# Optimization experiments

Hardware: AMD Instinct MI355X
Metric: run time of the kernel (lower is better)

Reference implementation:

```python
import jax, jax.numpy as jnp
import numpy as np

BLK = 128            # weight_block_size for w8a16 blockwise dequant
H = 1024             # hidden_size
I = 512              # moe_intermediate_size
E = 64               # n_routed_experts
T = 512              # tokens (seq_len)
K = 6                # num_experts_per_tok
G = 8                # n_group
TG = 3               # topk_group
NSH = 2              # n_shared_experts
I2 = I * NSH         # shared expert intermediate size
ROUTED_SCALE = 2.5
NORM_TOPK = True


def dq(w_int8, scale, blk=BLK):
    """Blockwise w8a16 dequant: w [..., M, N] int8, scale [..., M/blk, N/blk] f32."""
    *lead, M, N = w_int8.shape
    w = w_int8.astype(scale.dtype).reshape(*lead, M // blk, blk, N // blk, blk)
    return (w * scale[..., :, None, :, None]).reshape(*lead, M, N)


def setup_inputs() -> dict:
    key = jax.random.key(0)
    ks = jax.random.split(key, 16)
    ri = lambda k, shp: jax.random.randint(k, shp, -8, 8, dtype=jnp.int8)
    rs = lambda k, shp: jax.random.uniform(k, shp, minval=0.01, maxval=0.03, dtype=jnp.float32)
    return {
        "x": jax.random.normal(ks[0], (T, H), jnp.float32),
        "gate_w": jax.random.normal(ks[1], (E, H), jnp.float32) * 0.02,  # router gate [E,H]
        "wg": ri(ks[2], (E, I, H)),  "sg": rs(ks[3], (E, I // BLK, H // BLK)),
        "wu": ri(ks[4], (E, I, H)),  "su": rs(ks[5], (E, I // BLK, H // BLK)),
        "wd": ri(ks[6], (E, I, H)),  "sd": rs(ks[7], (E, I // BLK, H // BLK)),  # down, transposed layout [I,H]
        "sh_wg": ri(ks[8], (I2, H)),  "sh_sg": rs(ks[9], (I2 // BLK, H // BLK)),
        "sh_wu": ri(ks[10], (I2, H)), "sh_su": rs(ks[11], (I2 // BLK, H // BLK)),
        "sh_wd": ri(ks[12], (I2, H)), "sh_sd": rs(ks[13], (I2 // BLK, H // BLK)),
    }


def _moe(x, gate_w, wg, sg, wu, su, wd, sd, sh_wg, sh_sg, sh_wu, sh_su, sh_wd, sh_sd):
    Tn = x.shape[0]
    # --- router: sigmoid scoring + group-limited top-k ---
    scores = jax.nn.sigmoid(x @ gate_w.T)                       # [T, E]
    gsz = E // G
    group_scores = scores.reshape(Tn, G, gsz).max(axis=-1)      # [T, G]
    _, gidx = jax.lax.top_k(group_scores, TG)                   # [T, TG]
    gmask = jax.nn.one_hot(gidx, G, dtype=scores.dtype).sum(1)  # [T, G]
    emask = jnp.repeat(gmask, gsz, axis=-1)                     # [T, E]
    masked = jnp.where(emask > 0, scores, -jnp.inf)
    w, idx = jax.lax.top_k(masked, K)                           # [T, K]
    if NORM_TOPK:
        w = w / (w.sum(-1, keepdims=True) + 1e-20)
    w = w * ROUTED_SCALE
    # per-token combine weights over experts
    comb = (jax.nn.one_hot(idx, E, dtype=x.dtype) * w[:, :, None]).sum(1)  # [T, E]

    # --- routed experts: dequantized silu-gated MLPs, masked dense combine ---
    Wg, Wu, Wd = dq(wg, sg), dq(wu, su), dq(wd, sd)             # [E, I, H]
    g = jnp.einsum('th,eih->eti', x, Wg)                        # [E, T, I]
    u = jnp.einsum('th,eih->eti', x, Wu)
    hmid = jax.nn.silu(g) * u
    y = jnp.einsum('eti,eih->eth', hmid, Wd)                    # [E, T, H]
    routed = jnp.einsum('eth,te->th', y, comb)                  # [T, H]

    # --- shared experts MLP ---
    Sg, Su, Sd = dq(sh_wg, sh_sg), dq(sh_wu, sh_su), dq(sh_wd, sh_sd)
    shared = (jax.nn.silu(x @ Sg.T) * (x @ Su.T)) @ Sd          # [T, H]
    return routed + shared


def reference(x, gate_w, wg, sg, wu, su, wd, sd, sh_wg, sh_sg, sh_wu, sh_su, sh_wd, sh_sd):
    return _moe(x, gate_w, wg, sg, wu, su, wd, sd,
                sh_wg, sh_sg, sh_wu, sh_su, sh_wd, sh_sd)
```

## Files before the change

kernel.cpp:

```cpp
#include <hip/hip_runtime.h>
#include <math.h>
#include <stdint.h>

#define T_   512
#define H_   1024
#define I_   512
#define E_   64
#define K_   6
#define G_   8
#define TG_  3
#define EB_  80

typedef _Float16 h8 __attribute__((ext_vector_type(8)));
typedef _Float16 h4v __attribute__((ext_vector_type(4)));
typedef _Float16 h2v __attribute__((ext_vector_type(2)));
typedef float    f4 __attribute__((ext_vector_type(4)));

__global__ __launch_bounds__(64) void router_k(
    const float* __restrict__ x, const float* __restrict__ gw,
    int* __restrict__ cnt, int* __restrict__ tlist,
    float* __restrict__ wrow, _Float16* __restrict__ xh)
{
  const int t   = blockIdx.x;
  const int tid = threadIdx.x;
  __shared__ float sx[H_];
  __shared__ float sc[E_];

  for (int h4 = tid; h4 < H_/4; h4 += 64)
    ((float4*)sx)[h4] = ((const float4*)(x + (size_t)t*H_))[h4];
  __syncthreads();

  for (int h4 = tid; h4 < H_/4; h4 += 64) {
    float4 v = ((const float4*)sx)[h4];
    h4v o = { (_Float16)v.x, (_Float16)v.y, (_Float16)v.z, (_Float16)v.w };
    *(h4v*)(xh + (size_t)t*H_ + h4*4) = o;
  }
  if (t < 16) {
    int s  = t*64 + tid;
    int e  = 64 + (s >> 9);
    int tt = s & 511;
    tlist[e*T_ + tt] = (tt << 13) | (3072 + s);
    wrow[3072 + s] = 1.0f;
    if (s == 0) { cnt[64] = T_; cnt[65] = T_; }
  }

  const float* wr = gw + (size_t)tid * H_;
  float acc = 0.f;
  for (int h = 0; h < H_; h += 4) {
    float4 xv = *(const float4*)(sx + h);
    float4 wv = *(const float4*)(wr + h);
    acc = fmaf(xv.x, wv.x, acc); acc = fmaf(xv.y, wv.y, acc);
    acc = fmaf(xv.z, wv.z, acc); acc = fmaf(xv.w, wv.w, acc);
  }
  sc[tid] = 1.f / (1.f + expf(-acc));
  __syncthreads();

  if (tid == 0) {
    float gs[G_];
    #pragma unroll
    for (int g = 0; g < G_; g++) {
      float m = sc[g*8];
      #pragma unroll
      for (int j = 1; j < 8; j++) m = fmaxf(m, sc[g*8+j]);
      gs[g] = m;
    }
    unsigned gp = 0;
    for (int r = 0; r < TG_; r++) {
      int best = 0; float bv = -1e30f;
      for (int g = 0; g < G_; g++)
        if (!((gp >> g) & 1) && gs[g] > bv) { bv = gs[g]; best = g; }
      gp |= 1u << best;
    }
    int   eidx[K_]; float ew[K_];
    unsigned long long em = 0ull;
    float wsum = 0.f;
    for (int r = 0; r < K_; r++) {
      int best = 0; float bv = -1e30f;
      for (int e = 0; e < E_; e++) {
        if (!((gp >> (e >> 3)) & 1)) continue;
        if ((em >> e) & 1ull) continue;
        if (sc[e] > bv) { bv = sc[e]; best = e; }
      }
      em |= 1ull << best; eidx[r] = best; ew[r] = bv; wsum += bv;
    }
    const float inv = 2.5f / (wsum + 1e-20f);
    for (int r = 0; r < K_; r++) {
      int e = eidx[r];
      int pos = atomicAdd(&cnt[e], 1);
      tlist[e*T_ + pos] = (t << 13) | (t*K_ + r);
      wrow[t*K_ + r] = ew[r] * inv;
    }
  }
}

__device__ __forceinline__ void eb_decode(int eb, const int* cnt,
                                          int& e, int& lo, int& hi) {
  if (eb < E_) { e = eb; lo = 0; hi = cnt[e]; }
  else { int q = (eb - E_) & 7; e = E_ + ((eb - E_) >> 3); lo = q*64; hi = lo + 64; }
}

__device__ __forceinline__ h4v cvt4i(int4 w, float s) {
  h4v t = { (_Float16)((float)w.x*s), (_Float16)((float)w.y*s),
            (_Float16)((float)w.z*s), (_Float16)((float)w.w*s) };
  return t;
}

#define NKT_G 32

#define GU_STEP(KT, WN)                                                       \
  do {                                                                        \
    asm volatile("s_waitcnt vmcnt(" #WN ") lgkmcnt(0)" ::: "memory");         \
    __builtin_amdgcn_sched_barrier(0);                                        \
    __builtin_amdgcn_s_barrier();                                             \
    __builtin_amdgcn_sched_barrier(0);                                        \
    if ((KT) + 1 < NKT_G)                                                     \
      *(h4v*)(wdst + (((KT)+1)&1)*2560) =                                     \
          cvt4i(Wr[((KT)+1)%3], sv[((KT)+1)>>2]);                             \
    if ((KT) + 3 < NKT_G)                                                     \
      Wr[((KT)+3)%3] = *(const int4*)(wsrc + ((KT)+3)*32);                    \
    {                                                                         \
      const _Float16* tb = lds0 + ((KT)&1)*2560;                              \
      h8 bg = *(const h8*)(tb + ro0);                                         \
      h8 bu = *(const h8*)(tb + 1280 + ro0);                                  \
      accg = __builtin_amdgcn_mfma_f32_16x16x32_f16(Ar[(KT)%4], bg, accg, 0,0,0); \
      accu = __builtin_amdgcn_mfma_f32_16x16x32_f16(Ar[(KT)%4], bu, accu, 0,0,0); \
    }                                                                         \
    if ((KT) + 3 < NKT_G)                                                     \
      Ar[((KT)+3)%4] = *(const h8*)(ax + ((KT)+3)*32);                        \
  } while (0)

__global__ __launch_bounds__(512, 8) void gateup_k(
    const _Float16* __restrict__ xh,
    const int* __restrict__ wg, const float* __restrict__ sg,
    const int* __restrict__ wu, const float* __restrict__ su,
    const int* __restrict__ shwg, const float* __restrict__ shsg,
    const int* __restrict__ shwu, const float* __restrict__ shsu,
    const int* __restrict__ cnt, const int* __restrict__ tlist,
    const float* __restrict__ wrow,
    _Float16* __restrict__ hmid)
{
  const int bi = blockIdx.x;
  const int eb = blockIdx.y;
  int e, lo, hi;
  eb_decode(eb, cnt, e, lo, hi);
  if (hi <= lo) return;

  const int tid  = threadIdx.x;
  const int lane = tid & 63;
  const int wv   = tid >> 6;
  const int mr   = lane & 15;
  const int quad = lane >> 4;
  const int wm   = wv & 3;
  const int wn   = wv >> 2;

  const int *wgb, *wub; const float *sgp, *sup; int sib;
  if (e < E_) {
    wgb = wg + (size_t)e*I_*H_;  wub = wu + (size_t)e*I_*H_;
    sgp = sg + e*32;  sup = su + e*32;  sib = bi >> 2;
  } else {
    int hf = e - E_;
    wgb = shwg + (size_t)hf*512*H_;  wub = shwu + (size_t)hf*512*H_;
    sgp = shsg;  sup = shsu;  sib = hf*4 + (bi >> 2);
  }

  const int smat = tid >> 8;
  const int sr   = (tid >> 3) & 31;
  const int seg  = tid & 7;
  const int* wsrc = (smat ? wub : wgb) + (size_t)(bi*32 + sr)*H_ + seg*4;
  const float* ssc = (smat ? sup : sgp) + sib*8;
  float sv[8];
  #pragma unroll
  for (int b = 0; b < 8; b++) sv[b] = ssc[b];

  __shared__ _Float16 wlds[2*2*32*40];
  __shared__ int stok[64]; __shared__ int srw[64]; __shared__ float swt[64];
  _Float16* lds0 = wlds;
  _Float16* wdst = wlds + smat*1280 + sr*40 + seg*4;
  const int ro0 = (wn*16 + mr)*40 + quad*8;

  int4 Wr[3];
  h8   Ar[4];

  for (int base = lo; base < hi; base += 64) {
    __syncthreads();
    if (tid < 64) {
      int slot = base + tid;
      if (slot < hi) {
        int ent = tlist[e*T_ + slot];
        stok[tid] = ent >> 13; srw[tid] = ent & 8191;
        swt[tid]  = wrow[ent & 8191];
      } else { stok[tid] = -1; srw[tid] = 0; swt[tid] = 0.f; }
    }
    __syncthreads();

    int tk = stok[wm*16 + mr]; if (tk < 0) tk = 0;
    const _Float16* ax = xh + (size_t)tk*H_ + quad*8;

    f4 accg = (f4){0.f,0.f,0.f,0.f}, accu = accg;

    Wr[0] = *(const int4*)(wsrc);        Ar[0] = *(const h8*)(ax);
    Wr[1] = *(const int4*)(wsrc + 32);   Ar[1] = *(const h8*)(ax + 32);
    Wr[2] = *(const int4*)(wsrc + 64);   Ar[2] = *(const h8*)(ax + 64);
    asm volatile("s_waitcnt vmcnt(5)" ::: "memory");
    __builtin_amdgcn_sched_barrier(0);
    *(h4v*)(wdst) = cvt4i(Wr[0], sv[0]);

    GU_STEP(0,3);  GU_STEP(1,3);  GU_STEP(2,3);  GU_STEP(3,3);
    GU_STEP(4,3);  GU_STEP(5,3);  GU_STEP(6,3);  GU_STEP(7,3);
    GU_STEP(8,3);  GU_STEP(9,3);  GU_STEP(10,3); GU_STEP(11,3);
    GU_STEP(12,3); GU_STEP(13,3); GU_STEP(14,3); GU_STEP(15,3);
    GU_STEP(16,3); GU_STEP(17,3); GU_STEP(18,3); GU_STEP(19,3);
    GU_STEP(20,3); GU_STEP(21,3); GU_STEP(22,3); GU_STEP(23,3);
    GU_STEP(24,3); GU_STEP(25,3); GU_STEP(26,3); GU_STEP(27,3);
    GU_STEP(28,3); GU_STEP(29,3); GU_STEP(30,1); GU_STEP(31,0);

    const int icol = bi*32 + wn*16 + mr;
    #pragma unroll
    for (int r = 0; r < 4; r++) {
      int sl = wm*16 + quad*4 + r;
      if (stok[sl] >= 0) {
        float wt = swt[sl];
        float g0 = accg[r];
        float m0 = g0 / (1.f + expf(-g0)) * accu[r] * wt;
        hmid[(size_t)srw[sl]*I_ + icol] = (_Float16)m0;
      }
    }
  }
}
#undef GU_STEP

#define NKT_D 16

#define DN_LDW(S, KT)                                                         \
  do {                                                                        \
    Wr[S][0] = *(const int2*)(dsrc + (size_t)((KT)*32 + 0)*H_);               \
    Wr[S][1] = *(const int2*)(dsrc + (size_t)((KT)*32 + 1)*H_);               \
  } while (0)

#define DN_WRITE(S, BUF, SC)                                                  \
  do {                                                                        \
    h2v v0 = { (_Float16)((float)Wr[S][0].x*(SC)),                            \
               (_Float16)((float)Wr[S][1].x*(SC)) };                          \
    h2v v1 = { (_Float16)((float)Wr[S][0].y*(SC)),                            \
               (_Float16)((float)Wr[S][1].y*(SC)) };                          \
    *(h2v*)(ddst0 + (BUF)*1280)      = v0;                                    \
    *(h2v*)(ddst0 + (BUF)*1280 + 40) = v1;                                    \
  } while (0)

#define DN_STEP(KT, WN)                                                       \
  do {                                                                        \
    asm volatile("s_waitcnt vmcnt(" #WN ") lgkmcnt(0)" ::: "memory");         \
    __builtin_amdgcn_sched_barrier(0);                                        \
    __builtin_amdgcn_s_barrier();                                             \
    __builtin_amdgcn_sched_barrier(0);                                        \
    if ((KT) + 1 < NKT_D) DN_WRITE(((KT)+1)%3, ((KT)+1)&1, scd[((KT)+1)>>2]); \
    if ((KT) + 3 < NKT_D) DN_LDW(((KT)+3)%3, (KT)+3);                         \
    {                                                                         \
      const _Float16* tb = lds0 + ((KT)&1)*1280;                              \
      h8 b0 = *(const h8*)(tb + ro0);                                         \
      h8 b1 = *(const h8*)(tb + ro1);                                         \
      tot0 = __builtin_amdgcn_mfma_f32_16x16x32_f16(Ar[(KT)%4], b0, tot0, 0,0,0); \
      tot1 = __builtin_amdgcn_mfma_f32_16x16x32_f16(Ar[(KT)%4], b1, tot1, 0,0,0); \
    }                                                                         \
    if ((KT) + 3 < NKT_D)                                                     \
      Ar[((KT)+3)%4] = *(const h8*)(ap + ((KT)+3)*32);                        \
  } while (0)

__global__ __launch_bounds__(256, 8) void down_k(
    const int* __restrict__ wd, const float* __restrict__ sd,
    const int* __restrict__ shwd, const float* __restrict__ shsd,
    const int* __restrict__ cnt, const int* __restrict__ tlist,
    const _Float16* __restrict__ hmid, float* __restrict__ scr)
{
  const int hc = blockIdx.x;
  const int eb = blockIdx.y;
  int e, lo, hi;
  eb_decode(eb, cnt, e, lo, hi);
  if (hi <= lo) return;

  const int tid  = threadIdx.x;
  const int lane = tid & 63;
  const int wv   = tid >> 6;
  const int mr   = lane & 15;
  const int quad = lane >> 4;

  const int* wb; const float* sdp; int sib0;
  if (e < E_) { wb = wd + (size_t)e*I_*H_;        sdp = sd + e*32;  sib0 = 0; }
  else { int hf = e - E_; wb = shwd + (size_t)hf*512*H_; sdp = shsd; sib0 = hf*4; }
  float scd[4];
  #pragma unroll
  for (int ib = 0; ib < 4; ib++) scd[ib] = sdp[(sib0+ib)*8 + (hc >> 2)];

  const int ig = tid >> 4;
  const int hp = tid & 15;
  const int* dsrc = wb + (size_t)(ig*2)*H_ + hc*32 + hp*2;

  __shared__ _Float16 wlds[2*32*40];
  __shared__ int stok[64]; __shared__ int srw[64];
  _Float16* lds0  = wlds;
  _Float16* ddst0 = wlds + (hp*2)*40 + ig*2;
  const int ro0 = (     mr)*40 + quad*8;
  const int ro1 = (16 + mr)*40 + quad*8;

  int2 Wr[3][2];
  h8   Ar[4];

  for (int base = lo; base < hi; base += 64) {
    __syncthreads();
    if (tid < 64) {
      int slot = base + tid;
      if (slot < hi) {
        int ent = tlist[e*T_ + slot];
        stok[tid] = ent >> 13; srw[tid] = ent & 8191;
      } else { stok[tid] = -1; srw[tid] = 0; }
    }
    __syncthreads();

    const _Float16* ap = hmid + (size_t)srw[wv*16 + mr]*I_ + quad*8;

    f4 tot0 = (f4){0.f,0.f,0.f,0.f}, tot1 = tot0;

    DN_LDW(0, 0); Ar[0] = *(const h8*)(ap);
    DN_LDW(1, 1); Ar[1] = *(const h8*)(ap + 32);
    DN_LDW(2, 2); Ar[2] = *(const h8*)(ap + 64);
    asm volatile("s_waitcnt vmcnt(7)" ::: "memory");
    __builtin_amdgcn_sched_barrier(0);
    DN_WRITE(0, 0, scd[0]);

    DN_STEP(0,4);  DN_STEP(1,4);  DN_STEP(2,4);  DN_STEP(3,4);
    DN_STEP(4,4);  DN_STEP(5,4);  DN_STEP(6,4);  DN_STEP(7,4);
    DN_STEP(8,4);  DN_STEP(9,4);  DN_STEP(10,4); DN_STEP(11,4);
    DN_STEP(12,4); DN_STEP(13,4); DN_STEP(14,1); DN_STEP(15,0);

    #pragma unroll
    for (int r = 0; r < 4; r++) {
      int sl = wv*16 + quad*4 + r;
      if (stok[sl] >= 0) {
        int t  = stok[sl];
        int sr = srw[sl];
        int rank = (sr < 3072) ? (sr - t*6) : (6 + ((sr - 3072) >> 9));
        float* dst = scr + (size_t)(t*8 + rank)*H_ + hc*32 + mr;
        dst[0]  = tot0[r];
        dst[16] = tot1[r];
      }
    }
  }
}
#undef DN_STEP
#undef DN_WRITE
#undef DN_LDW

__global__ __launch_bounds__(256) void combine_k(
    const float* __restrict__ scr, float* __restrict__ out)
{
  int i = blockIdx.x*256 + threadIdx.x;
  int t = i >> 8;
  int c = i & 255;
  const float4* base = (const float4*)(scr + (size_t)t*8*H_) + c;
  float4 s = base[0];
  #pragma unroll
  for (int r = 1; r < 8; r++) {
    float4 v = base[(size_t)r*(H_/4)];
    s.x += v.x; s.y += v.y; s.z += v.z; s.w += v.w;
  }
  ((float4*)out)[i] = s;
}

extern "C" void kernel_launch(void* const* d_in, const int* in_sizes, int n_in,
                              void* d_out, int out_size, void* d_ws, size_t ws_size,
                              hipStream_t stream) {
  (void)in_sizes; (void)n_in; (void)ws_size; (void)out_size;
  const float* x    = (const float*)d_in[0];
  const float* gw   = (const float*)d_in[1];
  const int*   wg   = (const int*  )d_in[2];
  const float* sg   = (const float*)d_in[3];
  const int*   wu   = (const int*  )d_in[4];
  const float* su   = (const float*)d_in[5];
  const int*   wd   = (const int*  )d_in[6];
  const float* sd   = (const float*)d_in[7];
  const int*   shwg = (const int*  )d_in[8];
  const float* shsg = (const float*)d_in[9];
  const int*   shwu = (const int*  )d_in[10];
  const float* shsu = (const float*)d_in[11];
  const int*   shwd = (const int*  )d_in[12];
  const float* shsd = (const float*)d_in[13];
  float* out = (float*)d_out;

  char* ws = (char*)d_ws;
  int*      cnt   = (int*     ) ws;
  int*      tlist = (int*     )(ws + 1024);
  float*    wrow  = (float*   )(ws + 136192);
  _Float16* hmid  = (_Float16*)(ws + 152576);
  _Float16* xh    = (_Float16*)(ws + 4346880);
  float*    scr   = (float*   )(ws + 5395456);

  hipMemsetAsync(cnt, 0, 1024, stream);
  router_k<<<T_, 64, 0, stream>>>(x, gw, cnt, tlist, wrow, xh);
  gateup_k<<<dim3(16, EB_), 512, 0, stream>>>(xh, wg, sg, wu, su,
                                              shwg, shsg, shwu, shsu,
                                              cnt, tlist, wrow, hmid);
  down_k<<<dim3(32, EB_), 256, 0, stream>>>(wd, sd, shwd, shsd,
                                            cnt, tlist, hmid, scr);
  combine_k<<<512, 256, 0, stream>>>(scr, out);
}
```

Measured before the change: 539.7 us.

## Load weights directly into MFMA B-fragments, drop LDS staging and barriers

Both expert GEMM kernels now have each lane load its own int8-as-int32 weight elements from global memory and dequantize them straight into the MFMA B operand in registers. This removes the LDS double buffer and the per-step block barriers. Each block now covers 16 output columns instead of 32, and the grids double to compensate. The cost is redundant weight loads across waves that share the same columns, plus strided scalar global loads in the down kernel, in exchange for no LDS traffic and no synchronization.

```diff
diff --git a/kernel.cpp b/kernel.cpp
--- a/kernel.cpp
+++ b/kernel.cpp
@@ -13,7 +13,6 @@
 
 typedef _Float16 h8 __attribute__((ext_vector_type(8)));
 typedef _Float16 h4v __attribute__((ext_vector_type(4)));
-typedef _Float16 h2v __attribute__((ext_vector_type(2)));
 typedef float    f4 __attribute__((ext_vector_type(4)));
 
 __global__ __launch_bounds__(64) void router_k(
@@ -99,37 +98,47 @@
   else { int q = (eb - E_) & 7; e = E_ + ((eb - E_) >> 3); lo = q*64; hi = lo + 64; }
 }
 
-__device__ __forceinline__ h4v cvt4i(int4 w, float s) {
-  h4v t = { (_Float16)((float)w.x*s), (_Float16)((float)w.y*s),
-            (_Float16)((float)w.z*s), (_Float16)((float)w.w*s) };
-  return t;
-}
+__device__ __forceinline__ h8 cvt8(int4 a, int4 b, float s) {
+  union { _Float16 f[8]; h8 v; } t;
+  t.f[0]=(_Float16)((float)a.x*s); t.f[1]=(_Float16)((float)a.y*s);
+  t.f[2]=(_Float16)((float)a.z*s); t.f[3]=(_Float16)((float)a.w*s);
+  t.f[4]=(_Float16)((float)b.x*s); t.f[5]=(_Float16)((float)b.y*s);
+  t.f[6]=(_Float16)((float)b.z*s); t.f[7]=(_Float16)((float)b.w*s);
+  return t.v;
+}
+
+__device__ __forceinline__ h8 cvt8s(const int* w, float s) {
+  union { _Float16 f[8]; h8 v; } t;
+  #pragma unroll
+  for (int j = 0; j < 8; j++) t.f[j] = (_Float16)((float)w[j]*s);
+  return t.v;
+}
+
+#define WAITN(N) do { asm volatile("s_waitcnt vmcnt(" #N ")" ::: "memory"); \
+                      __builtin_amdgcn_sched_barrier(0); } while (0)
 
 #define NKT_G 32
 
-#define GU_STEP(KT, WN)                                                       \
+#define GU_LD(SLOT, KT)                                                       \
   do {                                                                        \
-    asm volatile("s_waitcnt vmcnt(" #WN ") lgkmcnt(0)" ::: "memory");         \
-    __builtin_amdgcn_sched_barrier(0);                                        \
-    __builtin_amdgcn_s_barrier();                                             \
-    __builtin_amdgcn_sched_barrier(0);                                        \
-    if ((KT) + 1 < NKT_G)                                                     \
-      *(h4v*)(wdst + (((KT)+1)&1)*2560) =                                     \
-          cvt4i(Wr[((KT)+1)%3], sv[((KT)+1)>>2]);                             \
-    if ((KT) + 3 < NKT_G)                                                     \
-      Wr[((KT)+3)%3] = *(const int4*)(wsrc + ((KT)+3)*32);                    \
-    {                                                                         \
-      const _Float16* tb = lds0 + ((KT)&1)*2560;                              \
-      h8 bg = *(const h8*)(tb + ro0);                                         \
-      h8 bu = *(const h8*)(tb + 1280 + ro0);                                  \
-      accg = __builtin_amdgcn_mfma_f32_16x16x32_f16(Ar[(KT)%4], bg, accg, 0,0,0); \
-      accu = __builtin_amdgcn_mfma_f32_16x16x32_f16(Ar[(KT)%4], bu, accu, 0,0,0); \
-    }                                                                         \
-    if ((KT) + 3 < NKT_G)                                                     \
-      Ar[((KT)+3)%4] = *(const h8*)(ax + ((KT)+3)*32);                        \
+    Wg[SLOT][0] = *(const int4*)(wsg + (KT)*32);                              \
+    Wg[SLOT][1] = *(const int4*)(wsg + (KT)*32 + 4);                          \
+    Wu[SLOT][0] = *(const int4*)(wsu + (KT)*32);                              \
+    Wu[SLOT][1] = *(const int4*)(wsu + (KT)*32 + 4);                          \
+    Aa[SLOT]    = *(const h8*)(ax + (KT)*32);                                 \
   } while (0)
 
-__global__ __launch_bounds__(512, 8) void gateup_k(
+#define GU_CMP(SLOT, KT)                                                      \
+  do {                                                                        \
+    h8 bg = cvt8(Wg[SLOT][0], Wg[SLOT][1], sgp[sib8 + ((KT)>>2)]);            \
+    h8 bu = cvt8(Wu[SLOT][0], Wu[SLOT][1], sup[sib8 + ((KT)>>2)]);            \
+    accg = __builtin_amdgcn_mfma_f32_16x16x32_f16(Aa[SLOT], bg, accg, 0,0,0); \
+    accu = __builtin_amdgcn_mfma_f32_16x16x32_f16(Aa[SLOT], bu, accu, 0,0,0); \
+  } while (0)
+
+#define GU_STEP(KT) do { WAITN(5); GU_CMP((KT)&1, KT); GU_LD((KT)&1, (KT)+2); } while (0)
+
+__global__ __launch_bounds__(256, 6) void gateup_k(
     const _Float16* __restrict__ xh,
     const int* __restrict__ wg, const float* __restrict__ sg,
     const int* __restrict__ wu, const float* __restrict__ su,
@@ -150,36 +159,25 @@
   const int wv   = tid >> 6;
   const int mr   = lane & 15;
   const int quad = lane >> 4;
-  const int wm   = wv & 3;
-  const int wn   = wv >> 2;
-
-  const int *wgb, *wub; const float *sgp, *sup; int sib;
+
+  const int *wgb, *wub; const float *sgp, *sup; int sib8;
   if (e < E_) {
     wgb = wg + (size_t)e*I_*H_;  wub = wu + (size_t)e*I_*H_;
-    sgp = sg + e*32;  sup = su + e*32;  sib = bi >> 2;
+    sgp = sg + e*32;  sup = su + e*32;  sib8 = (bi >> 3)*8;
   } else {
     int hf = e - E_;
     wgb = shwg + (size_t)hf*512*H_;  wub = shwu + (size_t)hf*512*H_;
-    sgp = shsg;  sup = shsu;  sib = hf*4 + (bi >> 2);
-  }
-
-  const int smat = tid >> 8;
-  const int sr   = (tid >> 3) & 31;
-  const int seg  = tid & 7;
-  const int* wsrc = (smat ? wub : wgb) + (size_t)(bi*32 + sr)*H_ + seg*4;
-  const float* ssc = (smat ? sup : sgp) + sib*8;
-  float sv[8];
-  #pragma unroll
-  for (int b = 0; b < 8; b++) sv[b] = ssc[b];
-
-  __shared__ _Float16 wlds[2*2*32*40];
+    sgp = shsg;  sup = shsu;  sib8 = (hf*4 + (bi >> 3))*8;
+  }
+
+  const int irow = bi*16 + mr;
+  const int* wsg = wgb + (size_t)irow*H_ + quad*8;
+  const int* wsu = wub + (size_t)irow*H_ + quad*8;
+
   __shared__ int stok[64]; __shared__ int srw[64]; __shared__ float swt[64];
-  _Float16* lds0 = wlds;
-  _Float16* wdst = wlds + smat*1280 + sr*40 + seg*4;
-  const int ro0 = (wn*16 + mr)*40 + quad*8;
-
-  int4 Wr[3];
-  h8   Ar[4];
+
+  int4 Wg[2][2], Wu[2][2];
+  h8   Aa[2];
 
   for (int base = lo; base < hi; base += 64) {
     __syncthreads();
@@ -193,80 +191,59 @@
     }
     __syncthreads();
 
-    int tk = stok[wm*16 + mr]; if (tk < 0) tk = 0;
+    int tk = stok[wv*16 + mr]; if (tk < 0) tk = 0;
     const _Float16* ax = xh + (size_t)tk*H_ + quad*8;
 
     f4 accg = (f4){0.f,0.f,0.f,0.f}, accu = accg;
 
-    Wr[0] = *(const int4*)(wsrc);        Ar[0] = *(const h8*)(ax);
-    Wr[1] = *(const int4*)(wsrc + 32);   Ar[1] = *(const h8*)(ax + 32);
-    Wr[2] = *(const int4*)(wsrc + 64);   Ar[2] = *(const h8*)(ax + 64);
-    asm volatile("s_waitcnt vmcnt(5)" ::: "memory");
-    __builtin_amdgcn_sched_barrier(0);
-    *(h4v*)(wdst) = cvt4i(Wr[0], sv[0]);
-
-    GU_STEP(0,3);  GU_STEP(1,3);  GU_STEP(2,3);  GU_STEP(3,3);
-    GU_STEP(4,3);  GU_STEP(5,3);  GU_STEP(6,3);  GU_STEP(7,3);
-    GU_STEP(8,3);  GU_STEP(9,3);  GU_STEP(10,3); GU_STEP(11,3);
-    GU_STEP(12,3); GU_STEP(13,3); GU_STEP(14,3); GU_STEP(15,3);
-    GU_STEP(16,3); GU_STEP(17,3); GU_STEP(18,3); GU_STEP(19,3);
-    GU_STEP(20,3); GU_STEP(21,3); GU_STEP(22,3); GU_STEP(23,3);
-    GU_STEP(24,3); GU_STEP(25,3); GU_STEP(26,3); GU_STEP(27,3);
-    GU_STEP(28,3); GU_STEP(29,3); GU_STEP(30,1); GU_STEP(31,0);
-
-    const int icol = bi*32 + wn*16 + mr;
+    GU_LD(0, 0); GU_LD(1, 1);
+
+    GU_STEP(0);  GU_STEP(1);  GU_STEP(2);  GU_STEP(3);
+    GU_STEP(4);  GU_STEP(5);  GU_STEP(6);  GU_STEP(7);
+    GU_STEP(8);  GU_STEP(9);  GU_STEP(10); GU_STEP(11);
+    GU_STEP(12); GU_STEP(13); GU_STEP(14); GU_STEP(15);
+    GU_STEP(16); GU_STEP(17); GU_STEP(18); GU_STEP(19);
+    GU_STEP(20); GU_STEP(21); GU_STEP(22); GU_STEP(23);
+    GU_STEP(24); GU_STEP(25); GU_STEP(26); GU_STEP(27);
+    GU_STEP(28); GU_STEP(29);
+    WAITN(5); GU_CMP(0, 30);
+    WAITN(0); GU_CMP(1, 31);
+
+    const int icol = bi*16 + mr;
     #pragma unroll
     for (int r = 0; r < 4; r++) {
-      int sl = wm*16 + quad*4 + r;
+      int sl = wv*16 + quad*4 + r;
       if (stok[sl] >= 0) {
-        float wt = swt[sl];
         float g0 = accg[r];
-        float m0 = g0 / (1.f + expf(-g0)) * accu[r] * wt;
+        float m0 = g0 / (1.f + expf(-g0)) * accu[r] * swt[sl];
         hmid[(size_t)srw[sl]*I_ + icol] = (_Float16)m0;
       }
     }
   }
 }
 #undef GU_STEP
+#undef GU_CMP
+#undef GU_LD
 
 #define NKT_D 16
 
-#define DN_LDW(S, KT)                                                         \
+#define DN_LD(SLOT, KT)                                                       \
   do {                                                                        \
-    Wr[S][0] = *(const int2*)(dsrc + (size_t)((KT)*32 + 0)*H_);               \
-    Wr[S][1] = *(const int2*)(dsrc + (size_t)((KT)*32 + 1)*H_);               \
+    _Pragma("unroll")                                                         \
+    for (int j = 0; j < 8; j++)                                               \
+      Wd[SLOT][j] = dsrc[(size_t)((KT)*32 + j)*H_];                           \
+    Aa[SLOT] = *(const h8*)(ap + (KT)*32);                                    \
   } while (0)
 
-#define DN_WRITE(S, BUF, SC)                                                  \
+#define DN_CMP(SLOT, KT)                                                      \
   do {                                                                        \
-    h2v v0 = { (_Float16)((float)Wr[S][0].x*(SC)),                            \
-               (_Float16)((float)Wr[S][1].x*(SC)) };                          \
-    h2v v1 = { (_Float16)((float)Wr[S][0].y*(SC)),                            \
-               (_Float16)((float)Wr[S][1].y*(SC)) };                          \
-    *(h2v*)(ddst0 + (BUF)*1280)      = v0;                                    \
-    *(h2v*)(ddst0 + (BUF)*1280 + 40) = v1;                                    \
+    h8 bf = cvt8s(Wd[SLOT], sdp[(sib0 + ((KT)>>2))*8 + hcb]);                 \
+    tot0 = __builtin_amdgcn_mfma_f32_16x16x32_f16(Aa[SLOT], bf, tot0, 0,0,0); \
   } while (0)
 
-#define DN_STEP(KT, WN)                                                       \
-  do {                                                                        \
-    asm volatile("s_waitcnt vmcnt(" #WN ") lgkmcnt(0)" ::: "memory");         \
-    __builtin_amdgcn_sched_barrier(0);                                        \
-    __builtin_amdgcn_s_barrier();                                             \
-    __builtin_amdgcn_sched_barrier(0);                                        \
-    if ((KT) + 1 < NKT_D) DN_WRITE(((KT)+1)%3, ((KT)+1)&1, scd[((KT)+1)>>2]); \
-    if ((KT) + 3 < NKT_D) DN_LDW(((KT)+3)%3, (KT)+3);                         \
-    {                                                                         \
-      const _Float16* tb = lds0 + ((KT)&1)*1280;                              \
-      h8 b0 = *(const h8*)(tb + ro0);                                         \
-      h8 b1 = *(const h8*)(tb + ro1);                                         \
-      tot0 = __builtin_amdgcn_mfma_f32_16x16x32_f16(Ar[(KT)%4], b0, tot0, 0,0,0); \
-      tot1 = __builtin_amdgcn_mfma_f32_16x16x32_f16(Ar[(KT)%4], b1, tot1, 0,0,0); \
-    }                                                                         \
-    if ((KT) + 3 < NKT_D)                                                     \
-      Ar[((KT)+3)%4] = *(const h8*)(ap + ((KT)+3)*32);                        \
-  } while (0)
-
-__global__ __launch_bounds__(256, 8) void down_k(
+#define DN_STEP(KT) do { WAITN(9); DN_CMP((KT)&1, KT); DN_LD((KT)&1, (KT)+2); } while (0)
+
+__global__ __launch_bounds__(256, 6) void down_k(
     const int* __restrict__ wd, const float* __restrict__ sd,
     const int* __restrict__ shwd, const float* __restrict__ shsd,
     const int* __restrict__ cnt, const int* __restrict__ tlist,
@@ -287,23 +264,14 @@
   const int* wb; const float* sdp; int sib0;
   if (e < E_) { wb = wd + (size_t)e*I_*H_;        sdp = sd + e*32;  sib0 = 0; }
   else { int hf = e - E_; wb = shwd + (size_t)hf*512*H_; sdp = shsd; sib0 = hf*4; }
-  float scd[4];
-  #pragma unroll
-  for (int ib = 0; ib < 4; ib++) scd[ib] = sdp[(sib0+ib)*8 + (hc >> 2)];
-
-  const int ig = tid >> 4;
-  const int hp = tid & 15;
-  const int* dsrc = wb + (size_t)(ig*2)*H_ + hc*32 + hp*2;
-
-  __shared__ _Float16 wlds[2*32*40];
+  const int hcb = hc >> 3;
+
+  const int* dsrc = wb + (size_t)(quad*8)*H_ + hc*16 + mr;
+
   __shared__ int stok[64]; __shared__ int srw[64];
-  _Float16* lds0  = wlds;
-  _Float16* ddst0 = wlds + (hp*2)*40 + ig*2;
-  const int ro0 = (     mr)*40 + quad*8;
-  const int ro1 = (16 + mr)*40 + quad*8;
-
-  int2 Wr[3][2];
-  h8   Ar[4];
+
+  int Wd[2][8];
+  h8  Aa[2];
 
   for (int base = lo; base < hi; base += 64) {
     __syncthreads();
@@ -318,19 +286,16 @@
 
     const _Float16* ap = hmid + (size_t)srw[wv*16 + mr]*I_ + quad*8;
 
-    f4 tot0 = (f4){0.f,0.f,0.f,0.f}, tot1 = tot0;
-
-    DN_LDW(0, 0); Ar[0] = *(const h8*)(ap);
-    DN_LDW(1, 1); Ar[1] = *(const h8*)(ap + 32);
-    DN_LDW(2, 2); Ar[2] = *(const h8*)(ap + 64);
-    asm volatile("s_waitcnt vmcnt(7)" ::: "memory");
-    __builtin_amdgcn_sched_barrier(0);
-    DN_WRITE(0, 0, scd[0]);
-
-    DN_STEP(0,4);  DN_STEP(1,4);  DN_STEP(2,4);  DN_STEP(3,4);
-    DN_STEP(4,4);  DN_STEP(5,4);  DN_STEP(6,4);  DN_STEP(7,4);
-    DN_STEP(8,4);  DN_STEP(9,4);  DN_STEP(10,4); DN_STEP(11,4);
-    DN_STEP(12,4); DN_STEP(13,4); DN_STEP(14,1); DN_STEP(15,0);
+    f4 tot0 = (f4){0.f,0.f,0.f,0.f};
+
+    DN_LD(0, 0); DN_LD(1, 1);
+
+    DN_STEP(0);  DN_STEP(1);  DN_STEP(2);  DN_STEP(3);
+    DN_STEP(4);  DN_STEP(5);  DN_STEP(6);  DN_STEP(7);
+    DN_STEP(8);  DN_STEP(9);  DN_STEP(10); DN_STEP(11);
+    DN_STEP(12); DN_STEP(13);
+    WAITN(9); DN_CMP(0, 14);
+    WAITN(0); DN_CMP(1, 15);
 
     #pragma unroll
     for (int r = 0; r < 4; r++) {
@@ -339,16 +304,14 @@
         int t  = stok[sl];
         int sr = srw[sl];
         int rank = (sr < 3072) ? (sr - t*6) : (6 + ((sr - 3072) >> 9));
-        float* dst = scr + (size_t)(t*8 + rank)*H_ + hc*32 + mr;
-        dst[0]  = tot0[r];
-        dst[16] = tot1[r];
+        scr[(size_t)(t*8 + rank)*H_ + hc*16 + mr] = tot0[r];
       }
     }
   }
 }
 #undef DN_STEP
-#undef DN_WRITE
-#undef DN_LDW
+#undef DN_CMP
+#undef DN_LD
 
 __global__ __launch_bounds__(256) void combine_k(
     const float* __restrict__ scr, float* __restrict__ out)
@@ -396,10 +359,10 @@
 
   hipMemsetAsync(cnt, 0, 1024, stream);
   router_k<<<T_, 64, 0, stream>>>(x, gw, cnt, tlist, wrow, xh);
-  gateup_k<<<dim3(16, EB_), 512, 0, stream>>>(xh, wg, sg, wu, su,
+  gateup_k<<<dim3(32, EB_), 256, 0, stream>>>(xh, wg, sg, wu, su,
                                               shwg, shsg, shwu, shsu,
                                               cnt, tlist, wrow, hmid);
-  down_k<<<dim3(32, EB_), 256, 0, stream>>>(wd, sd, shwd, shsd,
+  down_k<<<dim3(64, EB_), 256, 0, stream>>>(wd, sd, shwd, shsd,
                                             cnt, tlist, hmid, scr);
   combine_k<<<512, 256, 0, stream>>>(scr, out);
 }
```

Measured after the change: 1.115 ms. 107% more time.
